# Performance work log

Hardware: AMD Instinct MI355X
Metric: run time of the kernel (lower is better)

Reference implementation:

```python
import jax, jax.numpy as jnp
import numpy as np

NEG = -1000000.0  # same finite mask value as the Triton kernel


def setup_inputs() -> dict:
    key = jax.random.key(0)
    k1, k2, k3, k4 = jax.random.split(key, 4)
    B, H, KVH, S, D = 1, 32, 8, 2048, 128
    return {
        "q": jax.random.normal(k1, (B, H, S, D), dtype=jnp.float32),
        "k": jax.random.normal(k2, (B, KVH, S, D), dtype=jnp.float32),
        "v": jax.random.normal(k3, (B, KVH, S, D), dtype=jnp.float32),
        "sinks": jax.random.normal(k4, (H,), dtype=jnp.float32),
        "bandwidth": 1024,
    }


def reference(q, k, v, sinks, bandwidth):
    """Prefill flash attention with causal + sliding-window masking, GQA, and
    per-head attention sinks (extra logit in the softmax denominator)."""
    B, H, S, D = q.shape
    ratio = H // k.shape[1]  # KV_HEAD_RATIO
    kf = jnp.repeat(k, ratio, axis=1)  # [B,H,S,D]
    vf = jnp.repeat(v, ratio, axis=1)
    sm_scale = 1.0 / np.sqrt(D).astype(np.float32)

    logits = jnp.einsum("bhqd,bhkd->bhqk", q, kf) * sm_scale  # [B,H,S,S]
    q_pos = jnp.arange(S)[:, None]
    k_pos = jnp.arange(S)[None, :]
    mask = k_pos > q_pos  # causal
    if bandwidth > 0:
        mask = mask | (k_pos < q_pos - bandwidth + 1)  # sliding window
    logits = jnp.where(mask, NEG, logits)

    sink = sinks[None, :, None]  # [1,H,1] broadcast over batch, query
    m = jnp.maximum(jnp.max(logits, axis=-1), sink)  # [B,H,S]
    p = jnp.exp(logits - m[..., None])
    denom = p.sum(axis=-1) + jnp.exp(sink - m)  # sink contributes to denom only
    out = jnp.einsum("bhqk,bhkd->bhqd", p, vf) / denom[..., None]
    return out
```

## Files before the change

### kernel.cpp

```cpp
#include <hip/hip_runtime.h>
#include <hip/hip_bf16.h>

typedef __bf16 bf16x8 __attribute__((ext_vector_type(8)));
typedef unsigned short u16x8 __attribute__((ext_vector_type(8)));
typedef unsigned int u32x4 __attribute__((ext_vector_type(4)));
typedef float f32x16 __attribute__((ext_vector_type(16)));

#define SLEN 2048
#define DDIM 128
#define NH   32
#define NKVH 8
#define KVB  32
#define MINIT  -1e30f
#define MASKED -3e30f
#define LOG2E  1.4426950408889634f

static __device__ __forceinline__ unsigned short f2bfu(float f) {
  union { float f; unsigned u; } x; x.f = f;
  return (unsigned short)((x.u + 0x7fffu + ((x.u >> 16) & 1u)) >> 16);
}
static __device__ __forceinline__ float bfu2f(unsigned short u) {
  union { unsigned u; float f; } x; x.u = ((unsigned)u) << 16;
  return x.f;
}
static __device__ __forceinline__ unsigned cvt_pk_bf16(float lo, float hi) {
  unsigned r;
  asm("v_cvt_pk_bf16_f32 %0, %1, %2" : "=v"(r) : "v"(lo), "v"(hi));
  return r;
}
static __device__ __forceinline__ f32x16 mfma32(u16x8 a, u16x8 b, f32x16 c) {
  return __builtin_amdgcn_mfma_f32_32x32x16_bf16(
      __builtin_bit_cast(bf16x8, a), __builtin_bit_cast(bf16x8, b), c, 0, 0, 0);
}
static __device__ __forceinline__ void plswap(unsigned &a, unsigned &b) {
  asm volatile("v_permlane32_swap_b32 %0, %1" : "+v"(a), "+v"(b));
}

__global__ __launch_bounds__(256) void conv_kv(const float* __restrict__ k,
                                               const float* __restrict__ v,
                                               unsigned* __restrict__ kdst,
                                               unsigned short* __restrict__ vt) {
  __shared__ unsigned T32[32][17];
  const int bb = blockIdx.x;
  if (bb < 1024) {
    const int i = bb * 256 + threadIdx.x;
    const float4 f0 = ((const float4*)k)[2 * i];
    const float4 f1 = ((const float4*)k)[2 * i + 1];
    u32x4 o = { cvt_pk_bf16(f0.x, f0.y), cvt_pk_bf16(f0.z, f0.w),
                cvt_pk_bf16(f1.x, f1.y), cvt_pk_bf16(f1.z, f1.w) };
    ((u32x4*)kdst)[i] = o;
    return;
  }
  const int b   = bb - 1024;
  const int dt  = b & 3;
  const int st  = (b >> 2) & 63;
  const int kvh = b >> 8;
  const int r  = threadIdx.x >> 3;
  const int cg = threadIdx.x & 7;
  const float4 f = *(const float4*)(v + ((size_t)(kvh * SLEN + st * 32 + r) * DDIM) + dt * 32 + cg * 4);
  T32[r][cg * 2]     = cvt_pk_bf16(f.x, f.y);
  T32[r][cg * 2 + 1] = cvt_pk_bf16(f.z, f.w);
  __syncthreads();
  const int dr = threadIdx.x >> 3;
  const unsigned sel = (dr & 1) ? 0x07060302u : 0x05040100u;
  const unsigned a0 = T32[cg * 4 + 0][dr >> 1], a1 = T32[cg * 4 + 1][dr >> 1];
  const unsigned a2 = T32[cg * 4 + 2][dr >> 1], a3 = T32[cg * 4 + 3][dr >> 1];
  unsigned short* vp = vt + (size_t)kvh * DDIM * SLEN + (size_t)(dt * 32 + dr) * SLEN + st * 32 + cg * 4;
  const unsigned w0 = __builtin_amdgcn_perm(a1, a0, sel);
  const unsigned w1 = __builtin_amdgcn_perm(a3, a2, sel);
  vp[0] = (unsigned short)(w0 & 0xffff);
  vp[1] = (unsigned short)(w0 >> 16);
  vp[2] = (unsigned short)(w1 & 0xffff);
  vp[3] = (unsigned short)(w1 >> 16);
}

template <int NCH>
__global__ __launch_bounds__(256, 2) void attn_fwd(
    const float* __restrict__ q, const unsigned short* __restrict__ kbf,
    const unsigned short* __restrict__ vtg, const float* __restrict__ sinks,
    const int* __restrict__ bwp, float* __restrict__ out,
    unsigned short* __restrict__ pO, float* __restrict__ pm,
    float* __restrict__ pl) {
  constexpr int QBLK = 128;
  constexpr int NQT  = SLEN / QBLK;
  __shared__ unsigned short Kt[16 * 32 * 8];
  __shared__ unsigned short Vt2[4 * 128 * 8];
  __shared__ float SmS[4][32];

  const int tid  = threadIdx.x;
  const int wid  = tid >> 6;
  const int lane = tid & 63;
  const int qc   = lane & 31;
  const int hf   = lane >> 5;

  const int B   = blockIdx.x;
  const int x   = B & 7;
  const int j   = B >> 3;
  constexpr int per = 4 * NCH;
  const int qt  = NQT - 1 - (j / per);
  const int rem = j % per;
  const int hh  = rem / NCH;
  const int c   = rem % NCH;
  const int h   = x * 4 + hh;
  const int kvh = x;
  const int q0  = qt * QBLK;
  const int qrow0 = q0 + wid * 32;
  const int qpos  = qrow0 + qc;

  const int bwv    = bwp[0];
  const int lo_off = (bwv > 0) ? (bwv - 1) : SLEN;

  const int T0 = max(0, q0 - lo_off) >> 5;
  const int T1 = (q0 + QBLK - 1) >> 5;
  const int N  = T1 - T0 + 1;
  const int ch = (N + NCH - 1) / NCH;
  const int Ts = T0 + c * ch;
  const int Te = min(T1, Ts + ch - 1);

  const float c2 = 0.08838834764831845f * LOG2E;

  u16x8 qf[8];
  {
    const float* qp = q + ((size_t)(h * SLEN + qpos) * DDIM) + hf * 8;
    #pragma unroll
    for (int dk = 0; dk < 8; ++dk) {
      float4 f0 = *(const float4*)(qp + dk * 16);
      float4 f1 = *(const float4*)(qp + dk * 16 + 4);
      u32x4 t = { cvt_pk_bf16(f0.x, f0.y), cvt_pk_bf16(f0.z, f0.w),
                  cvt_pk_bf16(f1.x, f1.y), cvt_pk_bf16(f1.z, f1.w) };
      qf[dk] = __builtin_bit_cast(u16x8, t);
    }
  }

  float m2 = MINIT;
  float l_ln = 0.0f;
  f32x16 oacc[4];
  #pragma unroll
  for (int t = 0; t < 4; ++t)
    #pragma unroll
    for (int r = 0; r < 16; ++r) oacc[t][r] = 0.0f;

  const unsigned short* Kg = kbf + (size_t)kvh * SLEN * DDIM;
  const unsigned short* Vg = vtg + (size_t)kvh * DDIM * SLEN;

  const int i0 = tid, i1 = 256 + tid;
  const int ks0 = i0 >> 5, kr0 = i0 & 31;
  const int ks1 = i1 >> 5, kr1 = i1 & 31;
  const int vs0 = i0 >> 7, vd0 = i0 & 127;
  const int vs1 = i1 >> 7, vd1 = i1 & 127;
  const int klo0 = ks0 * 256 + kr0 * 8, klo1 = ks1 * 256 + kr1 * 8;
  const int vlo0 = vs0 * 1024 + vd0 * 8, vlo1 = vs1 * 1024 + vd1 * 8;

  int kro[8];
  #pragma unroll
  for (int dk = 0; dk < 8; ++dk) kro[dk] = (dk * 2 + hf) * 256 + qc * 8;

  if (Ts <= Te) {
    const int kbS = Ts * 32, kbE = Te * 32;

    u16x8 pk0, pk1, pv0, pv1;
    pk0 = *(const u16x8*)(Kg + (size_t)(kbS + kr0) * DDIM + ks0 * 8);
    pk1 = *(const u16x8*)(Kg + (size_t)(kbS + kr1) * DDIM + ks1 * 8);
    pv0 = *(const u16x8*)(Vg + (size_t)vd0 * SLEN + kbS + vs0 * 8);
    pv1 = *(const u16x8*)(Vg + (size_t)vd1 * SLEN + kbS + vs1 * 8);

    for (int kb = kbS; kb <= kbE; kb += KVB) {
      __syncthreads();
      *(u16x8*)&Kt[klo0]  = pk0;
      *(u16x8*)&Kt[klo1]  = pk1;
      *(u16x8*)&Vt2[vlo0] = pv0;
      *(u16x8*)&Vt2[vlo1] = pv1;
      __syncthreads();

      {
        const int nb = min(kb + KVB, kbE);
        pk0 = *(const u16x8*)(Kg + (size_t)(nb + kr0) * DDIM + ks0 * 8);
        pk1 = *(const u16x8*)(Kg + (size_t)(nb + kr1) * DDIM + ks1 * 8);
        pv0 = *(const u16x8*)(Vg + (size_t)vd0 * SLEN + nb + vs0 * 8);
        pv1 = *(const u16x8*)(Vg + (size_t)vd1 * SLEN + nb + vs1 * 8);
      }

      if (kb > qrow0 + 31) continue;
      if (kb + KVB - 1 < qrow0 - lo_off) continue;

      f32x16 sacc;
      #pragma unroll
      for (int r = 0; r < 16; ++r) sacc[r] = 0.0f;
      __builtin_amdgcn_s_setprio(1);
      #pragma unroll
      for (int dk = 0; dk < 8; ++dk)
        sacc = mfma32(*(const u16x8*)&Kt[kro[dk]], qf[dk], sacc);
      __builtin_amdgcn_s_setprio(0);

      float p[16];
      const bool interior = (kb + KVB - 1 <= qrow0) && (kb >= qrow0 + 31 - lo_off);
      if (interior) {
        #pragma unroll
        for (int r = 0; r < 16; ++r) p[r] = sacc[r] * c2;
      } else {
        #pragma unroll
        for (int rq = 0; rq < 4; ++rq)
          #pragma unroll
          for (int ri = 0; ri < 4; ++ri) {
            const int r  = rq * 4 + ri;
            const int kp = kb + ri + 8 * rq + 4 * hf;
            p[r] = ((kp <= qpos) && (kp >= qpos - lo_off)) ? sacc[r] * c2 : MASKED;
          }
      }

      float mx = p[0];
      #pragma unroll
      for (int r = 1; r < 16; ++r) mx = fmaxf(mx, p[r]);
      mx = fmaxf(mx, __shfl_xor(mx, 32));

      if (__any(mx > m2 + 11.5415605f)) {
        const float mn   = fmaxf(m2, mx);
        const float corr = exp2f(m2 - mn);
        l_ln *= corr;
        m2 = mn;
        if (hf == 0) SmS[wid][qc] = corr;
        #pragma unroll
        for (int r = 0; r < 16; ++r) {
          const float cr = SmS[wid][(r & 3) + 8 * (r >> 2) + 4 * hf];
          #pragma unroll
          for (int t = 0; t < 4; ++t) oacc[t][r] *= cr;
        }
      }

      float s = 0.0f;
      #pragma unroll
      for (int r = 0; r < 16; ++r) { p[r] = exp2f(p[r] - m2); s += p[r]; }
      l_ln += s;

      unsigned A0 = cvt_pk_bf16(p[0],  p[1]),  A1 = cvt_pk_bf16(p[2],  p[3]);
      unsigned B0 = cvt_pk_bf16(p[4],  p[5]),  B1 = cvt_pk_bf16(p[6],  p[7]);
      unsigned C0 = cvt_pk_bf16(p[8],  p[9]),  C1 = cvt_pk_bf16(p[10], p[11]);
      unsigned D0 = cvt_pk_bf16(p[12], p[13]), D1 = cvt_pk_bf16(p[14], p[15]);
      plswap(A0, B0); plswap(A1, B1);
      plswap(C0, D0); plswap(C1, D1);
      const u16x8 a0 = __builtin_bit_cast(u16x8, u32x4{A0, A1, B0, B1});
      const u16x8 a1 = __builtin_bit_cast(u16x8, u32x4{C0, C1, D0, D1});

      __builtin_amdgcn_s_setprio(1);
      #pragma unroll
      for (int t = 0; t < 4; ++t) {
        const u16x8 vb0 = *(const u16x8*)&Vt2[(0 * 2 + hf) * 1024 + (t * 32 + qc) * 8];
        oacc[t] = mfma32(a0, vb0, oacc[t]);
        const u16x8 vb1 = *(const u16x8*)&Vt2[(1 * 2 + hf) * 1024 + (t * 32 + qc) * 8];
        oacc[t] = mfma32(a1, vb1, oacc[t]);
      }
      __builtin_amdgcn_s_setprio(0);
    }
  }

  l_ln += __shfl_xor(l_ln, 32);

  if (NCH == 1) {
    const float sk2 = sinks[h] * LOG2E;
    const float M  = fmaxf(m2, sk2);
    const float ed = exp2f(m2 - M);
    const float fac = ed / (l_ln * ed + exp2f(sk2 - M));
    if (hf == 0) SmS[wid][qc] = fac;
    __builtin_amdgcn_s_barrier();
    #pragma unroll
    for (int r = 0; r < 16; ++r) {
      const int qr = (r & 3) + 8 * (r >> 2) + 4 * hf;
      const float fr = SmS[wid][qr];
      float* op = out + ((size_t)(h * SLEN + qrow0 + qr) * DDIM) + qc;
      #pragma unroll
      for (int t = 0; t < 4; ++t) op[t * 32] = oacc[t][r] * fr;
    }
  } else {
    const size_t Lb = ((size_t)(h * NQT + qt)) * NCH + c;
    if (hf == 0) {
      pm[Lb * QBLK + wid * 32 + qc] = m2;
      pl[Lb * QBLK + wid * 32 + qc] = l_ln;
    }
    #pragma unroll
    for (int r = 0; r < 16; ++r) {
      const int qr = (r & 3) + 8 * (r >> 2) + 4 * hf;
      unsigned short* po = pO + (Lb * QBLK + wid * 32 + qr) * 128 + qc;
      #pragma unroll
      for (int t = 0; t < 4; ++t) po[t * 32] = f2bfu(oacc[t][r]);
    }
  }
}

template <int NCH, int QBLK, int NQT>
__global__ __launch_bounds__(256) void mergeN(
    const unsigned short* __restrict__ pO, const float* __restrict__ pm,
    const float* __restrict__ pl, const float* __restrict__ sinks,
    float* __restrict__ out) {
  typedef unsigned short u16x8 __attribute__((ext_vector_type(8)));
  const int b   = blockIdx.x;
  const int x   = b & 7;
  const int jj2 = b >> 3;
  const int h   = x * 4 + (jj2 >> 5);
  const int sub = jj2 & 31;
  const int rloc = sub * 64 + (threadIdx.x >> 2);
  const int rid  = h * 2048 + rloc;
  const int d0   = (threadIdx.x & 3) * 32;
  const int qt   = rloc / QBLK;
  const int lr   = rloc % QBLK;
  const size_t base = ((size_t)(h * NQT + qt) * NCH) * QBLK + lr;
  const float sk2 = sinks[h] * LOG2E;
  float mc[NCH], lc[NCH];
  float M = sk2;
  #pragma unroll
  for (int c = 0; c < NCH; ++c) {
    mc[c] = pm[base + (size_t)c * QBLK];
    lc[c] = pl[base + (size_t)c * QBLK];
    M = fmaxf(M, mc[c]);
  }
  float denom = exp2f(sk2 - M);
  float sc[NCH];
  #pragma unroll
  for (int c = 0; c < NCH; ++c) { sc[c] = exp2f(mc[c] - M); denom += lc[c] * sc[c]; }
  const float inv = 1.0f / denom;
  float o[32];
  #pragma unroll
  for (int i = 0; i < 32; ++i) o[i] = 0.f;
  #pragma unroll
  for (int c = 0; c < NCH; ++c) {
    const unsigned short* pp = pO + (base + (size_t)c * QBLK) * 128 + d0;
    const float s = sc[c] * inv;
    #pragma unroll
    for (int i = 0; i < 4; ++i) {
      u16x8 a = *(const u16x8*)(pp + i * 8);
      #pragma unroll
      for (int jj = 0; jj < 8; ++jj) o[i*8+jj] += bfu2f(a[jj]) * s;
    }
  }
  float* op = out + (size_t)rid * 128 + d0;
  #pragma unroll
  for (int i = 0; i < 8; ++i)
    *(float4*)(op + i*4) = make_float4(o[i*4], o[i*4+1], o[i*4+2], o[i*4+3]);
}

extern "C" void kernel_launch(void* const* d_in, const int* in_sizes, int n_in,
                              void* d_out, int out_size, void* d_ws, size_t ws_size,
                              hipStream_t stream) {
  const float* q     = (const float*)d_in[0];
  const float* k     = (const float*)d_in[1];
  const float* v     = (const float*)d_in[2];
  const float* sinks = (const float*)d_in[3];
  const int*   bw    = (const int*)d_in[4];
  float* out = (float*)d_out;

  const size_t kvElems = (size_t)NKVH * SLEN * DDIM;
  unsigned short* kbf = (unsigned short*)d_ws;
  unsigned short* vtg = kbf + kvElems;
  unsigned short* pO  = vtg + kvElems;

  const size_t nPart2 = (size_t)NH * 16 * 2 * 128;
  const size_t need2  = 4 * kvElems + nPart2 * 128 * 2 + nPart2 * 8;

  conv_kv<<<dim3(1024 + NKVH * 64 * 4), 256, 0, stream>>>(k, v, (unsigned*)kbf, vtg);

  if (ws_size >= need2) {
    float* pm = (float*)(pO + nPart2 * 128);
    float* pl = pm + nPart2;
    attn_fwd<2><<<dim3(1024), 256, 0, stream>>>(q, kbf, vtg, sinks, bw, out, pO, pm, pl);
    mergeN<2, 128, 16><<<dim3(1024), 256, 0, stream>>>(pO, pm, pl, sinks, out);
  } else {
    attn_fwd<1><<<dim3(512), 256, 0, stream>>>(q, kbf, vtg, sinks, bw, out, pO, nullptr, nullptr);
  }
}
```

Baseline: 77.64 us.

## Double-buffer K/V tiles in LDS with direct global-to-LDS async loads

Replaces the register-staged K/V prefetch with `global_load_lds` DMA writes into a two-slot LDS buffer. The next tile loads into the alternate slot while the current one is consumed, so the loop needs one barrier per iteration instead of two. The launch-bounds occupancy hint rises from 2 to 3 blocks per CU, since the prefetch registers are gone. LDS use per block doubles, which could limit residency. Correctness depends on the barrier also waiting for the outstanding LDS-DMA loads.

```diff
diff --git a/kernel.cpp b/kernel.cpp
--- a/kernel.cpp
+++ b/kernel.cpp
@@ -34,6 +34,11 @@
 }
 static __device__ __forceinline__ void plswap(unsigned &a, unsigned &b) {
   asm volatile("v_permlane32_swap_b32 %0, %1" : "+v"(a), "+v"(b));
+}
+static __device__ __forceinline__ void gload16(const unsigned short* g, unsigned short* l) {
+  __builtin_amdgcn_global_load_lds(
+      (const __attribute__((address_space(1))) unsigned*)g,
+      (__attribute__((address_space(3))) unsigned*)l, 16, 0, 0);
 }
 
 __global__ __launch_bounds__(256) void conv_kv(const float* __restrict__ k,
@@ -75,7 +80,7 @@
 }
 
 template <int NCH>
-__global__ __launch_bounds__(256, 2) void attn_fwd(
+__global__ __launch_bounds__(256, 3) void attn_fwd(
     const float* __restrict__ q, const unsigned short* __restrict__ kbf,
     const unsigned short* __restrict__ vtg, const float* __restrict__ sinks,
     const int* __restrict__ bwp, float* __restrict__ out,
@@ -83,8 +88,8 @@
     float* __restrict__ pl) {
   constexpr int QBLK = 128;
   constexpr int NQT  = SLEN / QBLK;
-  __shared__ unsigned short Kt[16 * 32 * 8];
-  __shared__ unsigned short Vt2[4 * 128 * 8];
+  __shared__ unsigned short Kt[2][16 * 32 * 8];
+  __shared__ unsigned short Vt2[2][4 * 128 * 8];
   __shared__ float SmS[4][32];
 
   const int tid  = threadIdx.x;
@@ -143,13 +148,11 @@
   const unsigned short* Kg = kbf + (size_t)kvh * SLEN * DDIM;
   const unsigned short* Vg = vtg + (size_t)kvh * DDIM * SLEN;
 
-  const int i0 = tid, i1 = 256 + tid;
-  const int ks0 = i0 >> 5, kr0 = i0 & 31;
-  const int ks1 = i1 >> 5, kr1 = i1 & 31;
-  const int vs0 = i0 >> 7, vd0 = i0 & 127;
-  const int vs1 = i1 >> 7, vd1 = i1 & 127;
-  const int klo0 = ks0 * 256 + kr0 * 8, klo1 = ks1 * 256 + kr1 * 8;
-  const int vlo0 = vs0 * 1024 + vd0 * 8, vlo1 = vs1 * 1024 + vd1 * 8;
+  const int ks0 = tid >> 5,       kr0 = tid & 31;
+  const int ks1 = 8 + (tid >> 5), kr1 = tid & 31;
+  const int vs0 = tid >> 7,       vd0 = tid & 127;
+  const int vs1 = 2 + (tid >> 7), vd1 = tid & 127;
+  const int wb  = wid * 512;
 
   int kro[8];
   #pragma unroll
@@ -158,98 +161,98 @@
   if (Ts <= Te) {
     const int kbS = Ts * 32, kbE = Te * 32;
 
-    u16x8 pk0, pk1, pv0, pv1;
-    pk0 = *(const u16x8*)(Kg + (size_t)(kbS + kr0) * DDIM + ks0 * 8);
-    pk1 = *(const u16x8*)(Kg + (size_t)(kbS + kr1) * DDIM + ks1 * 8);
-    pv0 = *(const u16x8*)(Vg + (size_t)vd0 * SLEN + kbS + vs0 * 8);
-    pv1 = *(const u16x8*)(Vg + (size_t)vd1 * SLEN + kbS + vs1 * 8);
-
+    gload16(Kg + (size_t)(kbS + kr0) * DDIM + ks0 * 8, &Kt[0][wb]);
+    gload16(Kg + (size_t)(kbS + kr1) * DDIM + ks1 * 8, &Kt[0][2048 + wb]);
+    gload16(Vg + (size_t)vd0 * SLEN + kbS + vs0 * 8,   &Vt2[0][wb]);
+    gload16(Vg + (size_t)vd1 * SLEN + kbS + vs1 * 8,   &Vt2[0][2048 + wb]);
+
+    int cur = 0;
     for (int kb = kbS; kb <= kbE; kb += KVB) {
       __syncthreads();
-      *(u16x8*)&Kt[klo0]  = pk0;
-      *(u16x8*)&Kt[klo1]  = pk1;
-      *(u16x8*)&Vt2[vlo0] = pv0;
-      *(u16x8*)&Vt2[vlo1] = pv1;
-      __syncthreads();
-
-      {
-        const int nb = min(kb + KVB, kbE);
-        pk0 = *(const u16x8*)(Kg + (size_t)(nb + kr0) * DDIM + ks0 * 8);
-        pk1 = *(const u16x8*)(Kg + (size_t)(nb + kr1) * DDIM + ks1 * 8);
-        pv0 = *(const u16x8*)(Vg + (size_t)vd0 * SLEN + nb + vs0 * 8);
-        pv1 = *(const u16x8*)(Vg + (size_t)vd1 * SLEN + nb + vs1 * 8);
+
+      if (kb + KVB <= kbE) {
+        const int nb = kb + KVB;
+        const int nxt = cur ^ 1;
+        gload16(Kg + (size_t)(nb + kr0) * DDIM + ks0 * 8, &Kt[nxt][wb]);
+        gload16(Kg + (size_t)(nb + kr1) * DDIM + ks1 * 8, &Kt[nxt][2048 + wb]);
+        gload16(Vg + (size_t)vd0 * SLEN + nb + vs0 * 8,   &Vt2[nxt][wb]);
+        gload16(Vg + (size_t)vd1 * SLEN + nb + vs1 * 8,   &Vt2[nxt][2048 + wb]);
       }
 
-      if (kb > qrow0 + 31) continue;
-      if (kb + KVB - 1 < qrow0 - lo_off) continue;
-
-      f32x16 sacc;
-      #pragma unroll
-      for (int r = 0; r < 16; ++r) sacc[r] = 0.0f;
-      __builtin_amdgcn_s_setprio(1);
-      #pragma unroll
-      for (int dk = 0; dk < 8; ++dk)
-        sacc = mfma32(*(const u16x8*)&Kt[kro[dk]], qf[dk], sacc);
-      __builtin_amdgcn_s_setprio(0);
-
-      float p[16];
-      const bool interior = (kb + KVB - 1 <= qrow0) && (kb >= qrow0 + 31 - lo_off);
-      if (interior) {
-        #pragma unroll
-        for (int r = 0; r < 16; ++r) p[r] = sacc[r] * c2;
-      } else {
-        #pragma unroll
-        for (int rq = 0; rq < 4; ++rq)
+      const bool skip = (kb > qrow0 + 31) || (kb + KVB - 1 < qrow0 - lo_off);
+      if (!skip) {
+        const unsigned short* kbp = &Kt[cur][0];
+        const unsigned short* vbp = &Vt2[cur][0];
+
+        f32x16 sacc;
+        #pragma unroll
+        for (int r = 0; r < 16; ++r) sacc[r] = 0.0f;
+        __builtin_amdgcn_s_setprio(1);
+        #pragma unroll
+        for (int dk = 0; dk < 8; ++dk)
+          sacc = mfma32(*(const u16x8*)(kbp + kro[dk]), qf[dk], sacc);
+        __builtin_amdgcn_s_setprio(0);
+
+        float p[16];
+        const bool interior = (kb + KVB - 1 <= qrow0) && (kb >= qrow0 + 31 - lo_off);
+        if (interior) {
           #pragma unroll
-          for (int ri = 0; ri < 4; ++ri) {
-            const int r  = rq * 4 + ri;
-            const int kp = kb + ri + 8 * rq + 4 * hf;
-            p[r] = ((kp <= qpos) && (kp >= qpos - lo_off)) ? sacc[r] * c2 : MASKED;
+          for (int r = 0; r < 16; ++r) p[r] = sacc[r] * c2;
+        } else {
+          #pragma unroll
+          for (int rq = 0; rq < 4; ++rq)
+            #pragma unroll
+            for (int ri = 0; ri < 4; ++ri) {
+              const int r  = rq * 4 + ri;
+              const int kp = kb + ri + 8 * rq + 4 * hf;
+              p[r] = ((kp <= qpos) && (kp >= qpos - lo_off)) ? sacc[r] * c2 : MASKED;
+            }
+        }
+
+        float mx = p[0];
+        #pragma unroll
+        for (int r = 1; r < 16; ++r) mx = fmaxf(mx, p[r]);
+        mx = fmaxf(mx, __shfl_xor(mx, 32));
+
+        if (__any(mx > m2 + 11.5415605f)) {
+          const float mn   = fmaxf(m2, mx);
+          const float corr = exp2f(m2 - mn);
+          l_ln *= corr;
+          m2 = mn;
+          if (hf == 0) SmS[wid][qc] = corr;
+          #pragma unroll
+          for (int r = 0; r < 16; ++r) {
+            const float cr = SmS[wid][(r & 3) + 8 * (r >> 2) + 4 * hf];
+            #pragma unroll
+            for (int t = 0; t < 4; ++t) oacc[t][r] *= cr;
           }
+        }
+
+        float s = 0.0f;
+        #pragma unroll
+        for (int r = 0; r < 16; ++r) { p[r] = exp2f(p[r] - m2); s += p[r]; }
+        l_ln += s;
+
+        unsigned A0 = cvt_pk_bf16(p[0],  p[1]),  A1 = cvt_pk_bf16(p[2],  p[3]);
+        unsigned B0 = cvt_pk_bf16(p[4],  p[5]),  B1 = cvt_pk_bf16(p[6],  p[7]);
+        unsigned C0 = cvt_pk_bf16(p[8],  p[9]),  C1 = cvt_pk_bf16(p[10], p[11]);
+        unsigned D0 = cvt_pk_bf16(p[12], p[13]), D1 = cvt_pk_bf16(p[14], p[15]);
+        plswap(A0, B0); plswap(A1, B1);
+        plswap(C0, D0); plswap(C1, D1);
+        const u16x8 a0 = __builtin_bit_cast(u16x8, u32x4{A0, A1, B0, B1});
+        const u16x8 a1 = __builtin_bit_cast(u16x8, u32x4{C0, C1, D0, D1});
+
+        __builtin_amdgcn_s_setprio(1);
+        #pragma unroll
+        for (int t = 0; t < 4; ++t) {
+          const u16x8 vb0 = *(const u16x8*)(vbp + (0 * 2 + hf) * 1024 + (t * 32 + qc) * 8);
+          oacc[t] = mfma32(a0, vb0, oacc[t]);
+          const u16x8 vb1 = *(const u16x8*)(vbp + (1 * 2 + hf) * 1024 + (t * 32 + qc) * 8);
+          oacc[t] = mfma32(a1, vb1, oacc[t]);
+        }
+        __builtin_amdgcn_s_setprio(0);
       }
-
-      float mx = p[0];
-      #pragma unroll
-      for (int r = 1; r < 16; ++r) mx = fmaxf(mx, p[r]);
-      mx = fmaxf(mx, __shfl_xor(mx, 32));
-
-      if (__any(mx > m2 + 11.5415605f)) {
-        const float mn   = fmaxf(m2, mx);
-        const float corr = exp2f(m2 - mn);
-        l_ln *= corr;
-        m2 = mn;
-        if (hf == 0) SmS[wid][qc] = corr;
-        #pragma unroll
-        for (int r = 0; r < 16; ++r) {
-          const float cr = SmS[wid][(r & 3) + 8 * (r >> 2) + 4 * hf];
-          #pragma unroll
-          for (int t = 0; t < 4; ++t) oacc[t][r] *= cr;
-        }
-      }
-
-      float s = 0.0f;
-      #pragma unroll
-      for (int r = 0; r < 16; ++r) { p[r] = exp2f(p[r] - m2); s += p[r]; }
-      l_ln += s;
-
-      unsigned A0 = cvt_pk_bf16(p[0],  p[1]),  A1 = cvt_pk_bf16(p[2],  p[3]);
-      unsigned B0 = cvt_pk_bf16(p[4],  p[5]),  B1 = cvt_pk_bf16(p[6],  p[7]);
-      unsigned C0 = cvt_pk_bf16(p[8],  p[9]),  C1 = cvt_pk_bf16(p[10], p[11]);
-      unsigned D0 = cvt_pk_bf16(p[12], p[13]), D1 = cvt_pk_bf16(p[14], p[15]);
-      plswap(A0, B0); plswap(A1, B1);
-      plswap(C0, D0); plswap(C1, D1);
-      const u16x8 a0 = __builtin_bit_cast(u16x8, u32x4{A0, A1, B0, B1});
-      const u16x8 a1 = __builtin_bit_cast(u16x8, u32x4{C0, C1, D0, D1});
-
-      __builtin_amdgcn_s_setprio(1);
-      #pragma unroll
-      for (int t = 0; t < 4; ++t) {
-        const u16x8 vb0 = *(const u16x8*)&Vt2[(0 * 2 + hf) * 1024 + (t * 32 + qc) * 8];
-        oacc[t] = mfma32(a0, vb0, oacc[t]);
-        const u16x8 vb1 = *(const u16x8*)&Vt2[(1 * 2 + hf) * 1024 + (t * 32 + qc) * 8];
-        oacc[t] = mfma32(a1, vb1, oacc[t]);
-      }
-      __builtin_amdgcn_s_setprio(0);
+      cur ^= 1;
     }
   }
 
```

Result: slower. 81.10 us (+4.5%).
